# Kernel tuning notes

Hardware: AMD Instinct MI355X
Metric: run time of the kernel (lower is better)

## Reference

```python
import jax, jax.numpy as jnp
import numpy as np

DECAY = 0.99   # LIF membrane decay
INH = 1.625    # lateral inhibition strength (mode='max')


def setup_inputs() -> dict:
    key = jax.random.key(0)
    kx, kw = jax.random.split(key)
    B, Cin, Cout = 8192, 4096, 1024
    x = (jax.random.uniform(kx, (B, Cin)) < 0.2).astype(jnp.float32)
    # weights, then normweight(): clamp to [0,1] and scale each row so row-max == 0.1
    W = jax.random.uniform(kw, (Cout, Cin), dtype=jnp.float32)
    W = W / (W.max(axis=1, keepdims=True) / 0.1)
    return {"x": x, "W": W, "time_window": 10}


def reference(x, W, time_window):
    # current through the bias-free linear layer; constant across timesteps
    i = x @ W.T                                   # (B, Cout)
    # adaptive threshold init: threshold = 3 * max over batch (thre_init branch)
    thr = 3.0 * i.max(axis=0)                     # (Cout,)
    imax = i.max(axis=1, keepdims=True)           # (B, 1), for mode='max' inhibition
    C = i.shape[1]

    def step(mem, _):
        mem = mem * DECAY + i                     # LIF integration
        s = (mem > thr).astype(i.dtype)           # threshold fire
        mem = mem * (1.0 - s)                     # hard reset at all spikers
        row = s.max(axis=1, keepdims=True)        # (B,1) 1 if any neuron in row spiked
        # winner-take-all k=1: keep a single spiking neuron per row (first/argmax)
        wta = jax.nn.one_hot(jnp.argmax(s, axis=1), C, dtype=i.dtype) * row
        # lateral inhibition: subtract inh * max-current from losers in rows that spiked
        mem = mem - INH * imax * (row - wta)
        return mem, wta

    mem0 = jnp.zeros_like(i)
    _, wtas = jax.lax.scan(step, mem0, None, length=time_window)
    return wtas.sum(axis=0)                       # accumulated spikes (B, Cout)
```

## Files before the change

kernel.cpp:

```cpp
#include <hip/hip_runtime.h>
#include <cstdint>

#define B_DIM 8192
#define CIN   4096
#define COUT  1024

constexpr double W_SCALE   = 83230720.0;
constexpr int    QMAX      = 8323072;
constexpr double INV_SCALE = 0.1 / 8323072.0;

using i32x4 = __attribute__((ext_vector_type(4))) int;

__device__ __forceinline__ void async_copy16(void* lds, const void* g) {
    auto l = (__attribute__((address_space(3))) void*)(uintptr_t)(lds);
    auto p = (const __attribute__((address_space(1))) void*)(uintptr_t)(g);
    __builtin_amdgcn_global_load_lds(p, l, 16, 0, 0);
}

__global__ void prep_x(const float* __restrict__ x, int8_t* __restrict__ Ai) {
    const int idx = blockIdx.x * 256 + threadIdx.x;
    const float4* xp = (const float4*)x + (size_t)idx * 4;
    float4 v0 = xp[0], v1 = xp[1], v2 = xp[2], v3 = xp[3];
    auto pk = [](float a, float b, float c, float d) -> int {
        return (a != 0.f ? 1 : 0) | ((b != 0.f ? 1 : 0) << 8) |
               ((c != 0.f ? 1 : 0) << 16) | ((d != 0.f ? 1 : 0) << 24);
    };
    int4 r;
    r.x = pk(v0.x, v0.y, v0.z, v0.w);
    r.y = pk(v1.x, v1.y, v1.z, v1.w);
    r.z = pk(v2.x, v2.y, v2.z, v2.w);
    r.w = pk(v3.x, v3.y, v3.z, v3.w);
    ((int4*)Ai)[idx] = r;
}

__global__ void prep_w(const float* __restrict__ W, int8_t* __restrict__ Bd,
                       unsigned long long* __restrict__ cm) {
    const int idx = blockIdx.x * 256 + threadIdx.x;
    float4 w = ((const float4*)W)[idx];
    float ws[4] = {w.x, w.y, w.z, w.w};
    char dg[3][4];
#pragma unroll
    for (int k = 0; k < 4; ++k) {
        int qv = __double2int_rn((double)ws[k] * W_SCALE);
        qv = max(0, min(QMAX, qv));
        int d0 = ((qv + 128) & 255) - 128; int tq = (qv - d0) >> 8;
        int d1 = ((tq + 128) & 255) - 128; int d2 = (tq - d1) >> 8;
        dg[0][k] = (char)d0; dg[1][k] = (char)d1; dg[2][k] = (char)d2;
    }
    const size_t off = (size_t)idx * 4;
#pragma unroll
    for (int p = 0; p < 3; ++p) {
        char4 c4; c4.x = dg[p][0]; c4.y = dg[p][1]; c4.z = dg[p][2]; c4.w = dg[p][3];
        *(char4*)(Bd + (size_t)p * COUT * CIN + off) = c4;
    }
    if (idx < COUT) cm[idx] = 0ull;
}

template <int P>
__device__ __forceinline__ void mma16(const i32x4 (&a)[4], const i32x4 (&b)[4],
                                      i32x4 (&acc)[3][4][4]) {
    __builtin_amdgcn_s_setprio(1);
#pragma unroll
    for (int mi = 0; mi < 4; ++mi)
#pragma unroll
        for (int ni = 0; ni < 4; ++ni)
            acc[P][mi][ni] = __builtin_amdgcn_mfma_i32_16x16x64_i8(
                a[mi], b[ni], acc[P][mi][ni], 0, 0, 0);
    __builtin_amdgcn_s_setprio(0);
}

#define BAR()   __builtin_amdgcn_s_barrier()
#define LGKM0() asm volatile("s_waitcnt lgkmcnt(0)" ::: "memory")
#define VMW(n)  asm volatile("s_waitcnt vmcnt(" #n ")" ::: "memory")

__global__ __launch_bounds__(512, 2) void gemm_i8(const int8_t* __restrict__ A,
                                                  const int8_t* __restrict__ Bm,
                                                  double* __restrict__ Sc,
                                                  unsigned long long* __restrict__ cm) {
    __shared__ alignas(16) int8_t lds[131072];
    const int tid  = threadIdx.x;
    const int lane = tid & 63;
    const int wave = tid >> 6;

    const int wg = (int)blockIdx.x;
    const int bn = wg & 3;
    const int bm = wg >> 2;

    const int stid   = tid >> 3;
    const int cswz16 = ((tid & 7) ^ (stid & 7)) << 4;
    const int8_t* gA = A  + (size_t)(bm * 128 + stid) * CIN + cswz16;
    const int8_t* gB = Bm + (size_t)(bn * 256 + stid) * CIN + cswz16;
    const int wv1024 = wave << 10;

#define SA_(t_) do {                                                            \
    int8_t* d_ = lds + (((t_) & 1) << 14) + wv1024;                             \
    const int8_t* s_ = gA + ((t_) << 7);                                        \
    async_copy16(d_,        s_);                                                \
    async_copy16(d_ + 8192, s_ + (size_t)64 * CIN);                             \
} while (0)
#define SB_(t_, p_) do {                                                        \
    int8_t* d_ = lds + 32768 + ((p_) << 15) + wv1024;                           \
    const int8_t* s_ = gB + (size_t)(p_) * COUT * CIN + ((t_) << 7);            \
    async_copy16(d_,         s_);                                               \
    async_copy16(d_ + 8192,  s_ + (size_t)64  * CIN);                           \
    async_copy16(d_ + 16384, s_ + (size_t)128 * CIN);                           \
    async_copy16(d_ + 24576, s_ + (size_t)192 * CIN);                           \
} while (0)

    const int wr = wave >> 2, wc = wave & 3;
    const int fr = lane & 15;
    const int q  = lane >> 4;
    const int ck0 = (q ^ (fr & 7)) << 4;
    const int abase = (wr * 64 + fr) * 128;
    const int bbase = (wc * 64 + fr) * 128;

    i32x4 a[4], b[4];
    i32x4 acc[3][4][4] = {};

#define LDA_(t_, kk_) do {                                                      \
    const int8_t* p_ = lds + (((t_) & 1) << 14) + abase + (ck0 ^ ((kk_) * 64)); \
    a[0] = *(const i32x4*)(p_);        a[1] = *(const i32x4*)(p_ + 2048);       \
    a[2] = *(const i32x4*)(p_ + 4096); a[3] = *(const i32x4*)(p_ + 6144);       \
} while (0)
#define LDB_(p_, kk_) do {                                                      \
    const int8_t* q_ = lds + 32768 + ((p_) << 15) + bbase + (ck0 ^ ((kk_) * 64)); \
    b[0] = *(const i32x4*)(q_);        b[1] = *(const i32x4*)(q_ + 2048);       \
    b[2] = *(const i32x4*)(q_ + 4096); b[3] = *(const i32x4*)(q_ + 6144);       \
} while (0)

    SA_(0); SB_(0, 0); SB_(0, 1);
    VMW(4); BAR();

#pragma unroll 1
    for (int t = 0; t < 31; ++t) {
        LDA_(t, 0); LDB_(0, 0); SB_(t, 2); SA_(t + 1);
        BAR(); LGKM0(); mma16<0>(a, b, acc); VMW(6); BAR();
        LDB_(1, 0);
        BAR(); LGKM0(); mma16<1>(a, b, acc); VMW(2); BAR();
        LDB_(2, 0);
        BAR(); LGKM0(); mma16<2>(a, b, acc); BAR();
        LDA_(t, 1); LDB_(0, 1);
        BAR(); LGKM0(); mma16<0>(a, b, acc); BAR();
        LDB_(1, 1); SB_(t + 1, 0);
        BAR(); LGKM0(); mma16<1>(a, b, acc); BAR();
        LDB_(2, 1); SB_(t + 1, 1);
        BAR(); LGKM0(); mma16<2>(a, b, acc); VMW(4); BAR();
    }
    LDA_(31, 0); LDB_(0, 0); SB_(31, 2);
    BAR(); LGKM0(); mma16<0>(a, b, acc); VMW(4); BAR();
    LDB_(1, 0);
    BAR(); LGKM0(); mma16<1>(a, b, acc); VMW(0); BAR();
    LDB_(2, 0);
    BAR(); LGKM0(); mma16<2>(a, b, acc); BAR();
    LDA_(31, 1); LDB_(0, 1);
    BAR(); LGKM0(); mma16<0>(a, b, acc); BAR();
    LDB_(1, 1);
    BAR(); LGKM0(); mma16<1>(a, b, acc); BAR();
    LDB_(2, 1);
    BAR(); LGKM0(); mma16<2>(a, b, acc); BAR();

    const int gm0 = bm * 128 + wr * 64 + q * 4;
    const int gn0 = bn * 256 + wc * 64 + fr;
    double vmax[4] = {0.0, 0.0, 0.0, 0.0};
#pragma unroll
    for (int mi = 0; mi < 4; ++mi)
#pragma unroll
        for (int ni = 0; ni < 4; ++ni) {
            const int gn = gn0 + ni * 16;
#pragma unroll
            for (int reg = 0; reg < 4; ++reg) {
                const int gm = gm0 + mi * 16 + reg;
                long long isum = (long long)acc[0][mi][ni][reg]
                               + 256ll   * (long long)acc[1][mi][ni][reg]
                               + 65536ll * (long long)acc[2][mi][ni][reg];
                double v = (double)isum * INV_SCALE;
                Sc[(size_t)gm * COUT + gn] = v;
                vmax[ni] = fmax(vmax[ni], v);
            }
        }
#pragma unroll
    for (int ni = 0; ni < 4; ++ni) {
        vmax[ni] = fmax(vmax[ni], __shfl_xor(vmax[ni], 16, 64));
        vmax[ni] = fmax(vmax[ni], __shfl_xor(vmax[ni], 32, 64));
    }
    double* red = (double*)lds;
    if (lane < 16) {
#pragma unroll
        for (int ni = 0; ni < 4; ++ni)
            red[wave * 64 + ni * 16 + fr] = vmax[ni];
    }
    __syncthreads();
    if (tid < 256) {
        const int c = tid;
        const int wcq = c >> 6, nic = (c >> 4) & 3, frc = c & 15;
        double m = fmax(red[wcq * 64 + nic * 16 + frc],
                        red[(wcq + 4) * 64 + nic * 16 + frc]);
        atomicMax(cm + bn * 256 + c, (unsigned long long)__double_as_longlong(m));
    }
#undef SA_
#undef SB_
#undef LDA_
#undef LDB_
}

__global__ void scan_k(const double* __restrict__ Sc, const unsigned long long* __restrict__ cm,
                       const int* __restrict__ twp, float* __restrict__ out) {
    const int lane = threadIdx.x & 63;
    const int wave = threadIdx.x >> 6;
    const int b = blockIdx.x * 4 + wave;
    const int T = *twp;
    const double* row = Sc + (size_t)b * COUT;

    double iv[16], mem[16], thr[16];
    int cnt[16];
    double imax = 0.0;
#pragma unroll
    for (int u = 0; u < 16; ++u) {
        const int j = lane + u * 64;
        iv[u]  = row[j];
        thr[u] = 3.0 * __longlong_as_double((long long)cm[j]);
        mem[u] = 0.0; cnt[u] = 0;
        imax = fmax(imax, iv[u]);
    }
#pragma unroll
    for (int d = 32; d >= 1; d >>= 1) imax = fmax(imax, __shfl_xor(imax, d, 64));
    const double h = 1.625 * imax;

    for (int t = 0; t < T; ++t) {
        int first = 0x7fffffff;
        bool sp[16];
#pragma unroll
        for (int u = 0; u < 16; ++u) {
            mem[u] = mem[u] * 0.99 + iv[u];
            sp[u] = mem[u] > thr[u];
            if (sp[u]) first = min(first, lane + u * 64);
        }
#pragma unroll
        for (int d = 32; d >= 1; d >>= 1) first = min(first, __shfl_xor(first, d, 64));
        const bool rowspike = first < 0x7fffffff;
#pragma unroll
        for (int u = 0; u < 16; ++u) {
            if (sp[u]) mem[u] = 0.0;
            if (rowspike) {
                if (lane + u * 64 == first) cnt[u]++;
                else mem[u] -= h;
            }
        }
    }
#pragma unroll
    for (int u = 0; u < 16; ++u)
        out[(size_t)b * COUT + lane + u * 64] = (float)cnt[u];
}

extern "C" void kernel_launch(void* const* d_in, const int* in_sizes, int n_in,
                              void* d_out, int out_size, void* d_ws, size_t ws_size,
                              hipStream_t stream) {
    const float* x  = (const float*)d_in[0];
    const float* W  = (const float*)d_in[1];
    const int*   tw = (const int*)d_in[2];
    float* out = (float*)d_out;

    int8_t* Ai = (int8_t*)d_ws;
    int8_t* Bd = Ai + (size_t)B_DIM * CIN;
    double* Sc = (double*)(Bd + (size_t)3 * COUT * CIN);
    unsigned long long* cm =
        (unsigned long long*)((int8_t*)Sc + (size_t)B_DIM * COUT * 8);

    hipLaunchKernelGGL(prep_x,  dim3(8192), dim3(256), 0, stream, x, Ai);
    hipLaunchKernelGGL(prep_w,  dim3(4096), dim3(256), 0, stream, W, Bd, cm);
    hipLaunchKernelGGL(gemm_i8, dim3(256),  dim3(512), 0, stream, Ai, Bd, Sc, cm);
    hipLaunchKernelGGL(scan_k,  dim3(2048), dim3(256), 0, stream, Sc, cm, tw, out);
}
```

Baseline: 345.5 us.

## Double-buffer MFMA operand registers to overlap LDS reads with int8 MFMAs

Restructures the GEMM main loop so the A and B fragments for the next MFMA group are loaded from LDS into alternate register sets while the current group runs. Partial lgkmcnt waits and sched_barrier replace the full lgkmcnt(0) before each MFMA block, and the number of barriers per stage drops from two to one. The goal is to hide LDS read latency behind matrix ops. In exchange it uses more VGPRs, which could hurt the 2-waves/EU occupancy target. The vmcnt(0) waits are also stricter than the earlier partial counts, which may expose global-load latency.

```diff
diff --git a/kernel.cpp b/kernel.cpp
--- a/kernel.cpp
+++ b/kernel.cpp
@@ -56,22 +56,24 @@
     if (idx < COUT) cm[idx] = 0ull;
 }
 
-template <int P>
 __device__ __forceinline__ void mma16(const i32x4 (&a)[4], const i32x4 (&b)[4],
-                                      i32x4 (&acc)[3][4][4]) {
+                                      i32x4 (*accp)[4]) {
     __builtin_amdgcn_s_setprio(1);
 #pragma unroll
     for (int mi = 0; mi < 4; ++mi)
 #pragma unroll
         for (int ni = 0; ni < 4; ++ni)
-            acc[P][mi][ni] = __builtin_amdgcn_mfma_i32_16x16x64_i8(
-                a[mi], b[ni], acc[P][mi][ni], 0, 0, 0);
+            accp[mi][ni] = __builtin_amdgcn_mfma_i32_16x16x64_i8(
+                a[mi], b[ni], accp[mi][ni], 0, 0, 0);
     __builtin_amdgcn_s_setprio(0);
 }
 
-#define BAR()   __builtin_amdgcn_s_barrier()
-#define LGKM0() asm volatile("s_waitcnt lgkmcnt(0)" ::: "memory")
-#define VMW(n)  asm volatile("s_waitcnt vmcnt(" #n ")" ::: "memory")
+#define BAR()    __builtin_amdgcn_s_barrier()
+#define SCHED0() __builtin_amdgcn_sched_barrier(0)
+#define W0()     asm volatile("s_waitcnt lgkmcnt(0)" ::: "memory")
+#define W4()     asm volatile("s_waitcnt lgkmcnt(4)" ::: "memory")
+#define W8()     asm volatile("s_waitcnt lgkmcnt(8)" ::: "memory")
+#define VMW0()   asm volatile("s_waitcnt vmcnt(0)" ::: "memory")
 
 __global__ __launch_bounds__(512, 2) void gemm_i8(const int8_t* __restrict__ A,
                                                   const int8_t* __restrict__ Bm,
@@ -114,50 +116,51 @@
     const int abase = (wr * 64 + fr) * 128;
     const int bbase = (wc * 64 + fr) * 128;
 
-    i32x4 a[4], b[4];
+    i32x4 aK0[4], aK1[4], bA[4], bB[4];
     i32x4 acc[3][4][4] = {};
 
-#define LDA_(t_, kk_) do {                                                      \
+#define LDA_(dst_, t_, kk_) do {                                                \
     const int8_t* p_ = lds + (((t_) & 1) << 14) + abase + (ck0 ^ ((kk_) * 64)); \
-    a[0] = *(const i32x4*)(p_);        a[1] = *(const i32x4*)(p_ + 2048);       \
-    a[2] = *(const i32x4*)(p_ + 4096); a[3] = *(const i32x4*)(p_ + 6144);       \
-} while (0)
-#define LDB_(p_, kk_) do {                                                      \
+    dst_[0] = *(const i32x4*)(p_);        dst_[1] = *(const i32x4*)(p_ + 2048); \
+    dst_[2] = *(const i32x4*)(p_ + 4096); dst_[3] = *(const i32x4*)(p_ + 6144); \
+} while (0)
+#define LDB_(dst_, p_, kk_) do {                                                \
     const int8_t* q_ = lds + 32768 + ((p_) << 15) + bbase + (ck0 ^ ((kk_) * 64)); \
-    b[0] = *(const i32x4*)(q_);        b[1] = *(const i32x4*)(q_ + 2048);       \
-    b[2] = *(const i32x4*)(q_ + 4096); b[3] = *(const i32x4*)(q_ + 6144);       \
+    dst_[0] = *(const i32x4*)(q_);        dst_[1] = *(const i32x4*)(q_ + 2048); \
+    dst_[2] = *(const i32x4*)(q_ + 4096); dst_[3] = *(const i32x4*)(q_ + 6144); \
 } while (0)
 
     SA_(0); SB_(0, 0); SB_(0, 1);
-    VMW(4); BAR();
+    VMW0(); BAR();
+    LDB_(bB, 0, 0); LDA_(aK0, 0, 0);
 
 #pragma unroll 1
     for (int t = 0; t < 31; ++t) {
-        LDA_(t, 0); LDB_(0, 0); SB_(t, 2); SA_(t + 1);
-        BAR(); LGKM0(); mma16<0>(a, b, acc); VMW(6); BAR();
-        LDB_(1, 0);
-        BAR(); LGKM0(); mma16<1>(a, b, acc); VMW(2); BAR();
-        LDB_(2, 0);
-        BAR(); LGKM0(); mma16<2>(a, b, acc); BAR();
-        LDA_(t, 1); LDB_(0, 1);
-        BAR(); LGKM0(); mma16<0>(a, b, acc); BAR();
-        LDB_(1, 1); SB_(t + 1, 0);
-        BAR(); LGKM0(); mma16<1>(a, b, acc); BAR();
-        LDB_(2, 1); SB_(t + 1, 1);
-        BAR(); LGKM0(); mma16<2>(a, b, acc); VMW(4); BAR();
-    }
-    LDA_(31, 0); LDB_(0, 0); SB_(31, 2);
-    BAR(); LGKM0(); mma16<0>(a, b, acc); VMW(4); BAR();
-    LDB_(1, 0);
-    BAR(); LGKM0(); mma16<1>(a, b, acc); VMW(0); BAR();
-    LDB_(2, 0);
-    BAR(); LGKM0(); mma16<2>(a, b, acc); BAR();
-    LDA_(31, 1); LDB_(0, 1);
-    BAR(); LGKM0(); mma16<0>(a, b, acc); BAR();
-    LDB_(1, 1);
-    BAR(); LGKM0(); mma16<1>(a, b, acc); BAR();
-    LDB_(2, 1);
-    BAR(); LGKM0(); mma16<2>(a, b, acc); BAR();
+        LDB_(bA, 1, 0); SB_(t, 2);
+        W4(); SCHED0(); mma16(aK0, bB, acc[0]); VMW0(); BAR();
+        LDB_(bB, 2, 0); SA_(t + 1);
+        W4(); SCHED0(); mma16(aK0, bA, acc[1]); BAR();
+        LDB_(bA, 0, 1); LDA_(aK1, t, 1);
+        W8(); SCHED0(); mma16(aK0, bB, acc[2]); BAR();
+        LDB_(bB, 1, 1);
+        W4(); SCHED0(); mma16(aK1, bA, acc[0]); BAR();
+        LDB_(bA, 2, 1); SB_(t + 1, 0);
+        W4(); SCHED0(); mma16(aK1, bB, acc[1]); VMW0(); BAR();
+        LDB_(bB, 0, 0); LDA_(aK0, t + 1, 0); SB_(t + 1, 1);
+        W8(); SCHED0(); mma16(aK1, bA, acc[2]); VMW0(); BAR();
+    }
+    LDB_(bA, 1, 0); SB_(31, 2);
+    W4(); SCHED0(); mma16(aK0, bB, acc[0]); VMW0(); BAR();
+    LDB_(bB, 2, 0);
+    W4(); SCHED0(); mma16(aK0, bA, acc[1]); BAR();
+    LDB_(bA, 0, 1); LDA_(aK1, 31, 1);
+    W8(); SCHED0(); mma16(aK0, bB, acc[2]); BAR();
+    LDB_(bB, 1, 1);
+    W4(); SCHED0(); mma16(aK1, bA, acc[0]); BAR();
+    LDB_(bA, 2, 1);
+    W4(); SCHED0(); mma16(aK1, bB, acc[1]); BAR();
+    W0(); SCHED0(); mma16(aK1, bA, acc[2]);
+    BAR();
 
     const int gm0 = bm * 128 + wr * 64 + q * 4;
     const int gn0 = bn * 256 + wc * 64 + fr;
```

Result: slower. 559.6 us (+62.0%).
